# Performance work log

Measured on AMD Instinct MI355X. Metric: run time of the kernel, lower is better.

## Reference

```python
import jax, jax.numpy as jnp
import numpy as np

N_HEADS = 8
N_GROUPS = 32  # GroupNorm groups (normalization(channels) in guided-diffusion)
EPS = 1e-5


def setup_inputs() -> dict:
    key = jax.random.key(0)
    ks = jax.random.split(key, 7)
    b, c, hh, ww = 16, 512, 32, 32
    x = jax.random.normal(ks[0], (b, c, hh, ww), dtype=jnp.float32)
    norm_w = 1.0 + 0.02 * jax.random.normal(ks[1], (c,), dtype=jnp.float32)
    norm_b = 0.02 * jax.random.normal(ks[2], (c,), dtype=jnp.float32)
    # pointwise Conv1d == matmul over channels; note proj_out is zero-initialized
    # in the original, we use random weights so the op is non-trivial.
    qkv_w = jax.random.normal(ks[3], (3 * c, c), dtype=jnp.float32) / np.sqrt(c).astype(np.float32)
    qkv_b = 0.02 * jax.random.normal(ks[4], (3 * c,), dtype=jnp.float32)
    proj_w = jax.random.normal(ks[5], (c, c), dtype=jnp.float32) / np.sqrt(c).astype(np.float32)
    proj_b = 0.02 * jax.random.normal(ks[6], (c,), dtype=jnp.float32)
    return {"x": x, "norm_w": norm_w, "norm_b": norm_b,
            "qkv_w": qkv_w, "qkv_b": qkv_b, "proj_w": proj_w, "proj_b": proj_b}


def reference(x, norm_w, norm_b, qkv_w, qkv_b, proj_w, proj_b):
    b, c, hh, ww = x.shape
    t = hh * ww
    xf = x.reshape(b, c, t)

    # GroupNorm(32, c): normalize over (c//G channels, T) per group
    xg = xf.reshape(b, N_GROUPS, (c // N_GROUPS) * t)
    mu = jnp.mean(xg, axis=-1, keepdims=True)
    var = jnp.var(xg, axis=-1, keepdims=True)
    hn = ((xg - mu) * jax.lax.rsqrt(var + EPS)).reshape(b, c, t)
    hn = hn * norm_w[:, None] + norm_b[:, None]

    # pointwise conv: [b, 3c, t]
    qkv = jnp.einsum('oc,bct->bot', qkv_w, hn) + qkv_b[:, None]

    ch = c // N_HEADS
    qkv = qkv.reshape(b * N_HEADS, 3 * ch, t)
    q, k, v = jnp.split(qkv, 3, axis=1)  # each [b*H, ch, t]
    scale = np.float32(1.0 / np.sqrt(np.sqrt(ch)))
    w = jnp.einsum('bct,bcs->bts', q * scale, k * scale)  # [b*H, t, t]
    w = jax.nn.softmax(w.astype(jnp.float32), axis=-1).astype(qkv.dtype)
    a = jnp.einsum('bts,bcs->bct', w, v).reshape(b, c, t)

    h = jnp.einsum('oc,bct->bot', proj_w, a) + proj_b[:, None]
    return (xf + h).reshape(b, c, hh, ww)
```

## Files before the change

### kernel.cpp

```cpp
#include <hip/hip_runtime.h>

#define TPB 256

typedef __attribute__((ext_vector_type(8))) __bf16 bf16x8;
typedef __attribute__((ext_vector_type(4))) float f32x4;
typedef __attribute__((ext_vector_type(8))) unsigned short u16x8;
typedef __attribute__((ext_vector_type(4))) unsigned short u16x4;
typedef __attribute__((ext_vector_type(4))) unsigned int u32x4;
typedef __attribute__((ext_vector_type(2))) unsigned int u32x2;

typedef __attribute__((address_space(1))) const void gconst_void;
typedef __attribute__((address_space(3))) void lds_void;

__device__ __forceinline__ unsigned short f2bf(float f) {
  unsigned u = __builtin_bit_cast(unsigned, f);
  u += 0x7FFFu + ((u >> 16) & 1u);
  return (unsigned short)(u >> 16);
}

__device__ __forceinline__ float exp2_fast(float x) {
  float r;
  asm("v_exp_f32 %0, %1" : "=v"(r) : "v"(x));
  return r;
}

__device__ __forceinline__ float rcp_fast(float x) {
  float r;
  asm("v_rcp_f32 %0, %1" : "=v"(r) : "v"(x));
  return r;
}

__device__ __forceinline__ unsigned cvt_pk_bf16(float lo, float hi) {
  unsigned r;
  asm("v_cvt_pk_bf16_f32 %0, %1, %2" : "=v"(r) : "v"(lo), "v"(hi));
  return r;
}

__global__ void k_gn_stats(const float* __restrict__ x, float* __restrict__ mu,
                           float* __restrict__ rs) {
  int bg = blockIdx.x;
  const float4* p = reinterpret_cast<const float4*>(x + (size_t)bg * 16384);
  float s = 0.f, ss = 0.f;
  for (int i = threadIdx.x; i < 4096; i += TPB) {
    float4 v = p[i];
    s += v.x + v.y + v.z + v.w;
    ss += v.x * v.x + v.y * v.y + v.z * v.z + v.w * v.w;
  }
#pragma unroll
  for (int off = 1; off < 64; off <<= 1) {
    s += __shfl_xor(s, off, 64);
    ss += __shfl_xor(ss, off, 64);
  }
  __shared__ float rbuf[4][2];
  int wave = threadIdx.x >> 6;
  if ((threadIdx.x & 63) == 0) { rbuf[wave][0] = s; rbuf[wave][1] = ss; }
  __syncthreads();
  if (threadIdx.x == 0) {
    float S = 0.f, SS = 0.f;
    for (int i = 0; i < 4; ++i) { S += rbuf[i][0]; SS += rbuf[i][1]; }
    float m = S * (1.f / 16384.f);
    float var = SS * (1.f / 16384.f) - m * m;
    mu[bg] = m;
    rs[bg] = rsqrtf(var + 1e-5f);
  }
}

__global__ void k_gn_apply(const float* __restrict__ x, const float* __restrict__ mu,
                           const float* __restrict__ rs, const float* __restrict__ nw,
                           const float* __restrict__ nb, unsigned short* __restrict__ hnT) {
  __shared__ unsigned short tile[64][72];
  int b = blockIdx.z, ct = blockIdx.y, tt = blockIdx.x;
  int tid = threadIdx.x;
  int cloc = tid >> 2;
  int tseg = tid & 3;
  int c = ct * 64 + cloc;
  int g = c >> 4;
  float m = mu[b * 32 + g], r = rs[b * 32 + g];
  float a = r * nw[c];
  float bb = nb[c] - m * a;
  const float4* src = reinterpret_cast<const float4*>(
      x + ((size_t)(b * 512 + c)) * 1024 + tt * 64 + tseg * 16);
#pragma unroll
  for (int i = 0; i < 4; ++i) {
    float4 v = src[i];
    int tl = tseg * 16 + i * 4;
    tile[tl + 0][cloc] = f2bf(v.x * a + bb);
    tile[tl + 1][cloc] = f2bf(v.y * a + bb);
    tile[tl + 2][cloc] = f2bf(v.z * a + bb);
    tile[tl + 3][cloc] = f2bf(v.w * a + bb);
  }
  __syncthreads();
  int trow = tid >> 3;
  int cs = (tid & 7) * 8;
#pragma unroll
  for (int p = 0; p < 2; ++p) {
    int tr = trow + p * 32;
    u16x8 v8 = *reinterpret_cast<const u16x8*>(&tile[tr][cs]);
    *reinterpret_cast<u16x8*>(hnT + ((size_t)(b * 1024 + tt * 64 + tr)) * 512 + ct * 64 + cs) = v8;
  }
}

__global__ void k_f32_to_bf16(const float* __restrict__ src, unsigned short* __restrict__ dst,
                              int n4) {
  int i = blockIdx.x * blockDim.x + threadIdx.x;
  if (i < n4) {
    float4 v = reinterpret_cast<const float4*>(src)[i];
    u16x4 o;
    o[0] = f2bf(v.x); o[1] = f2bf(v.y); o[2] = f2bf(v.z); o[3] = f2bf(v.w);
    reinterpret_cast<u16x4*>(dst)[i] = o;
  }
}

__global__ __launch_bounds__(256) void k_qkv_gemm(
    const unsigned short* __restrict__ hnT, const unsigned short* __restrict__ wq,
    const float* __restrict__ qkv_b, unsigned short* __restrict__ Q,
    unsigned short* __restrict__ K, unsigned short* __restrict__ V) {
  __shared__ unsigned short As[2][4096];
  __shared__ unsigned short Bs[2][4096];
  int tid = threadIdx.x;
  int lane = tid & 63, wave = tid >> 6;
  int wm = wave >> 1, wn = wave & 1;
  int g = lane >> 4, li = lane & 15;

  int wg = blockIdx.x;
  int lin = (wg & 7) * 192 + (wg >> 3);
  int bx = lin % 12;
  int tmp = lin / 12;
  int by = tmp & 7;
  int b = tmp >> 3;
  int mbase = by * 128;
  int nbase = bx * 128;

  const unsigned short* Ag = hnT + (size_t)b * 1024 * 512 + (size_t)mbase * 512;
  const unsigned short* Bg = wq + (size_t)nbase * 512;

  int kq = (lane & 3) ^ ((lane >> 3) & 3);
  int rst = wave * 32 + (lane >> 2);
  const char* pA0 = (const char*)Ag + (size_t)rst * 1024 + kq * 16;
  const char* pA1 = pA0 + 16 * 1024;
  const char* pB0 = (const char*)Bg + (size_t)rst * 1024 + kq * 16;
  const char* pB1 = pB0 + 16 * 1024;
  int ldsA0 = wave * 1024, ldsA1 = wave * 1024 + 512;

  int voff = 32 * li + 8 * (g ^ ((li >> 1) & 3));

  f32x4 zero = {0.f, 0.f, 0.f, 0.f};
  f32x4 acc[4][4];
#pragma unroll
  for (int mi = 0; mi < 4; ++mi)
#pragma unroll
    for (int ni = 0; ni < 4; ++ni) acc[mi][ni] = zero;

#define GISSUE(k0, buf)                                                                  \
  do {                                                                                   \
    __builtin_amdgcn_global_load_lds((gconst_void*)(pA0 + (k0) * 2),                     \
                                     (lds_void*)&As[buf][ldsA0], 16, 0, 0);              \
    __builtin_amdgcn_global_load_lds((gconst_void*)(pA1 + (k0) * 2),                     \
                                     (lds_void*)&As[buf][ldsA1], 16, 0, 0);              \
    __builtin_amdgcn_global_load_lds((gconst_void*)(pB0 + (k0) * 2),                     \
                                     (lds_void*)&Bs[buf][ldsA0], 16, 0, 0);              \
    __builtin_amdgcn_global_load_lds((gconst_void*)(pB1 + (k0) * 2),                     \
                                     (lds_void*)&Bs[buf][ldsA1], 16, 0, 0);              \
  } while (0)

  GISSUE(0, 0);
#pragma unroll
  for (int kk = 0; kk < 16; ++kk) {
    asm volatile("s_waitcnt vmcnt(0)" ::: "memory");
    __builtin_amdgcn_s_barrier();
    asm volatile("" ::: "memory");
    if (kk < 15) GISSUE((kk + 1) * 32, (kk + 1) & 1);
    const int cur = kk & 1;
    bf16x8 af[4], bfr[4];
#pragma unroll
    for (int mi = 0; mi < 4; ++mi)
      af[mi] = *reinterpret_cast<const bf16x8*>(&As[cur][wm * 2048 + mi * 512 + voff]);
#pragma unroll
    for (int ni = 0; ni < 4; ++ni)
      bfr[ni] = *reinterpret_cast<const bf16x8*>(&Bs[cur][wn * 2048 + ni * 512 + voff]);
#pragma unroll
    for (int mi = 0; mi < 4; ++mi)
#pragma unroll
      for (int ni = 0; ni < 4; ++ni)
        acc[mi][ni] = __builtin_amdgcn_mfma_f32_16x16x32_bf16(af[mi], bfr[ni], acc[mi][ni], 0, 0, 0);
  }
#undef GISSUE

  const float SCALE = 0.42466090143f;
#pragma unroll
  for (int ni = 0; ni < 4; ++ni) {
    int o = nbase + wn * 64 + ni * 16 + li;
    int h = o / 192;
    int j = o - h * 192;
    int bh = b * 8 + h;
    float bias = qkv_b[o];
#pragma unroll
    for (int mi = 0; mi < 4; ++mi) {
      int t0 = mbase + wm * 64 + mi * 16 + g * 4;
      f32x4 v = acc[mi][ni];
      if (j < 64) {
#pragma unroll
        for (int r = 0; r < 4; ++r)
          Q[((size_t)bh * 1024 + t0 + r) * 64 + j] = f2bf((v[r] + bias) * SCALE);
      } else if (j < 128) {
#pragma unroll
        for (int r = 0; r < 4; ++r)
          K[((size_t)bh * 1024 + t0 + r) * 64 + (j - 64)] = f2bf((v[r] + bias) * SCALE);
      } else {
        u16x4 pv;
#pragma unroll
        for (int r = 0; r < 4; ++r) pv[r] = f2bf(v[r] + bias);
        *reinterpret_cast<u16x4*>(V + ((size_t)bh * 64 + (j - 128)) * 1024 + t0) = pv;
      }
    }
  }
}

__global__ __launch_bounds__(256) void k_attn(
    const unsigned short* __restrict__ Q, const unsigned short* __restrict__ K,
    const unsigned short* __restrict__ V, unsigned short* __restrict__ aT) {
  __shared__ unsigned short Kls[2][4096];
  __shared__ unsigned short Vls[2][4096];
  int tid = threadIdx.x;
  int lane = tid & 63, w = tid >> 6;
  int g = lane >> 4, li = lane & 15;

  int wg = blockIdx.x;
  int lin = (wg & 7) * 128 + (wg >> 3);
  int qt = lin & 7;
  int bh = lin >> 3;
  int tq0 = qt * 128;
  int b = bh >> 3, h = bh & 7;

  const unsigned short* Kg = K + (size_t)bh * 1024 * 64;
  const unsigned short* Vg = V + (size_t)bh * 64 * 1024;

  bf16x8 qf[2][2];
#pragma unroll
  for (int qi = 0; qi < 2; ++qi) {
    int t = tq0 + w * 32 + qi * 16 + li;
    const unsigned short* qp = Q + ((size_t)bh * 1024 + t) * 64 + g * 8;
    qf[qi][0] = *reinterpret_cast<const bf16x8*>(qp);
    qf[qi][1] = *reinterpret_cast<const bf16x8*>(qp + 32);
  }

  int r0 = w * 16 + (lane >> 3);
  int r1 = r0 + 8;
  int h0 = (r0 ^ (r0 >> 2)) & 7;
  int h1 = (r1 ^ (r1 >> 2)) & 7;
  int c0 = ((lane & 7) ^ h0) * 8;
  int c1 = ((lane & 7) ^ h1) * 8;
  const unsigned short* kg0 = Kg + (size_t)r0 * 64 + c0;
  const unsigned short* kg1 = Kg + (size_t)r1 * 64 + c1;
  const unsigned short* vg0 = Vg + (size_t)r0 * 1024 + c0;
  const unsigned short* vg1 = Vg + (size_t)r1 * 1024 + c1;

  int srowK = ((li >> 2) << 3) | (li & 3);

  f32x4 zero = {0.f, 0.f, 0.f, 0.f};
  f32x4 oacc[2][4];
  f32x4 l_acc[2];
#pragma unroll
  for (int qi = 0; qi < 2; ++qi) {
    l_acc[qi] = zero;
#pragma unroll
    for (int nj = 0; nj < 4; ++nj) oacc[qi][nj] = zero;
  }
  u32x4 onesw = {0x3F803F80u, 0x3F803F80u, 0x3F803F80u, 0x3F803F80u};
  bf16x8 ones = __builtin_bit_cast(bf16x8, onesw);

#define ISSUE(tt, pp)                                                                    \
  do {                                                                                   \
    __builtin_amdgcn_global_load_lds((gconst_void*)(kg0 + (size_t)(tt) * 4096),          \
                                     (lds_void*)&Kls[pp][w * 1024], 16, 0, 0);           \
    __builtin_amdgcn_global_load_lds((gconst_void*)(kg1 + (size_t)(tt) * 4096),          \
                                     (lds_void*)&Kls[pp][w * 1024 + 512], 16, 0, 0);     \
    __builtin_amdgcn_global_load_lds((gconst_void*)(vg0 + (size_t)(tt) * 64),            \
                                     (lds_void*)&Vls[pp][w * 1024], 16, 0, 0);           \
    __builtin_amdgcn_global_load_lds((gconst_void*)(vg1 + (size_t)(tt) * 64),            \
                                     (lds_void*)&Vls[pp][w * 1024 + 512], 16, 0, 0);     \
  } while (0)

#define ABODY(cur)                                                                        \
  do {                                                                                    \
    const unsigned short* kbase = &Kls[cur][0];                                           \
    const unsigned short* vbase = &Vls[cur][0];                                           \
    f32x4 sacc[2][4];                                                                     \
    _Pragma("unroll") for (int ni = 0; ni < 4; ++ni) {                                    \
      int rK = ((ni >> 1) << 5) + ((ni & 1) << 2) + srowK;                                \
      int hs = ((rK ^ (rK >> 2)) & 7) << 4;                                               \
      int off0 = ((g << 4)) ^ hs;                                                         \
      int off1 = (64 + (g << 4)) ^ hs;                                                    \
      bf16x8 kf0 = *reinterpret_cast<const bf16x8*>(&kbase[rK * 64 + (off0 >> 1)]);       \
      bf16x8 kf1 = *reinterpret_cast<const bf16x8*>(&kbase[rK * 64 + (off1 >> 1)]);       \
      _Pragma("unroll") for (int qi = 0; qi < 2; ++qi) {                                  \
        f32x4 s0 = __builtin_amdgcn_mfma_f32_16x16x32_bf16(kf0, qf[qi][0], zero, 0, 0, 0);\
        sacc[qi][ni] = __builtin_amdgcn_mfma_f32_16x16x32_bf16(kf1, qf[qi][1], s0, 0, 0, 0);\
      }                                                                                   \
    }                                                                                     \
    bf16x8 pfrag[2][2];                                                                   \
    _Pragma("unroll") for (int qi = 0; qi < 2; ++qi) {                                    \
      _Pragma("unroll") for (int ni = 0; ni < 4; ++ni)                                    \
        _Pragma("unroll") for (int r = 0; r < 4; ++r)                                     \
          sacc[qi][ni][r] = exp2_fast(sacc[qi][ni][r]);                                   \
      _Pragma("unroll") for (int kk = 0; kk < 2; ++kk) {                                  \
        u32x4 pw;                                                                         \
        pw[0] = cvt_pk_bf16(sacc[qi][2 * kk][0], sacc[qi][2 * kk][1]);                    \
        pw[1] = cvt_pk_bf16(sacc[qi][2 * kk][2], sacc[qi][2 * kk][3]);                    \
        pw[2] = cvt_pk_bf16(sacc[qi][2 * kk + 1][0], sacc[qi][2 * kk + 1][1]);            \
        pw[3] = cvt_pk_bf16(sacc[qi][2 * kk + 1][2], sacc[qi][2 * kk + 1][3]);            \
        pfrag[qi][kk] = __builtin_bit_cast(bf16x8, pw);                                   \
      }                                                                                   \
      l_acc[qi] = __builtin_amdgcn_mfma_f32_16x16x32_bf16(ones, pfrag[qi][0], l_acc[qi], 0, 0, 0); \
      l_acc[qi] = __builtin_amdgcn_mfma_f32_16x16x32_bf16(ones, pfrag[qi][1], l_acc[qi], 0, 0, 0); \
    }                                                                                     \
    _Pragma("unroll") for (int nj = 0; nj < 4; ++nj) {                                    \
      int rV = nj * 16 + li;                                                              \
      int hv = ((rV ^ (rV >> 2)) & 7) << 4;                                               \
      int off0 = ((g << 4)) ^ hv;                                                         \
      int off1 = (64 + (g << 4)) ^ hv;                                                    \
      bf16x8 vf0 = *reinterpret_cast<const bf16x8*>(&vbase[rV * 64 + (off0 >> 1)]);       \
      bf16x8 vf1 = *reinterpret_cast<const bf16x8*>(&vbase[rV * 64 + (off1 >> 1)]);       \
      _Pragma("unroll") for (int qi = 0; qi < 2; ++qi) {                                  \
        oacc[qi][nj] = __builtin_amdgcn_mfma_f32_16x16x32_bf16(vf0, pfrag[qi][0], oacc[qi][nj], 0, 0, 0); \
        oacc[qi][nj] = __builtin_amdgcn_mfma_f32_16x16x32_bf16(vf1, pfrag[qi][1], oacc[qi][nj], 0, 0, 0); \
      }                                                                                   \
    }                                                                                     \
  } while (0)

  ISSUE(0, 0);
  for (int t = 0; t < 16; ++t) {
    asm volatile("s_waitcnt vmcnt(0)" ::: "memory");
    __builtin_amdgcn_s_barrier();
    asm volatile("" ::: "memory");
    if (t < 15) ISSUE(t + 1, (t + 1) & 1);
    ABODY(t & 1);
  }
#undef ISSUE
#undef ABODY

#pragma unroll
  for (int qi = 0; qi < 2; ++qi) {
    float inv = rcp_fast(l_acc[qi][0]);
    int t = tq0 + w * 32 + qi * 16 + li;
#pragma unroll
    for (int nj = 0; nj < 4; ++nj) {
      u32x2 ov;
      ov[0] = cvt_pk_bf16(oacc[qi][nj][0] * inv, oacc[qi][nj][1] * inv);
      ov[1] = cvt_pk_bf16(oacc[qi][nj][2] * inv, oacc[qi][nj][3] * inv);
      *reinterpret_cast<u32x2*>(aT + ((size_t)b * 1024 + t) * 512 + h * 64 + nj * 16 + g * 4) = ov;
    }
  }
}

__global__ __launch_bounds__(256) void k_proj_gemm(
    const unsigned short* __restrict__ aT, const unsigned short* __restrict__ wp,
    const float* __restrict__ proj_b, const float* __restrict__ x,
    float* __restrict__ out) {
  __shared__ unsigned short As[2][4096];
  __shared__ unsigned short Bs[2][4096];
  int tid = threadIdx.x;
  int lane = tid & 63, wave = tid >> 6;
  int wm = wave >> 1, wn = wave & 1;
  int g = lane >> 4, li = lane & 15;

  int wg = blockIdx.x;
  int lin = (wg & 7) * 64 + (wg >> 3);
  int bx = lin & 7;
  int tmp = lin >> 3;
  int by = tmp & 3;
  int b = tmp >> 2;
  int mbase = by * 128;
  int nbase = bx * 128;

  const unsigned short* Ag = wp + (size_t)mbase * 512;
  const unsigned short* Bg = aT + (size_t)b * 1024 * 512 + (size_t)nbase * 512;

  int kq = (lane & 3) ^ ((lane >> 3) & 3);
  int rst = wave * 32 + (lane >> 2);
  const char* pA0 = (const char*)Ag + (size_t)rst * 1024 + kq * 16;
  const char* pA1 = pA0 + 16 * 1024;
  const char* pB0 = (const char*)Bg + (size_t)rst * 1024 + kq * 16;
  const char* pB1 = pB0 + 16 * 1024;
  int ldsA0 = wave * 1024, ldsA1 = wave * 1024 + 512;

  int voff = 32 * li + 8 * (g ^ ((li >> 1) & 3));

  f32x4 zero = {0.f, 0.f, 0.f, 0.f};
  f32x4 acc[4][4];
#pragma unroll
  for (int mi = 0; mi < 4; ++mi)
#pragma unroll
    for (int ni = 0; ni < 4; ++ni) acc[mi][ni] = zero;

#define GISSUE(k0, buf)                                                                  \
  do {                                                                                   \
    __builtin_amdgcn_global_load_lds((gconst_void*)(pA0 + (k0) * 2),                     \
                                     (lds_void*)&As[buf][ldsA0], 16, 0, 0);              \
    __builtin_amdgcn_global_load_lds((gconst_void*)(pA1 + (k0) * 2),                     \
                                     (lds_void*)&As[buf][ldsA1], 16, 0, 0);              \
    __builtin_amdgcn_global_load_lds((gconst_void*)(pB0 + (k0) * 2),                     \
                                     (lds_void*)&Bs[buf][ldsA0], 16, 0, 0);              \
    __builtin_amdgcn_global_load_lds((gconst_void*)(pB1 + (k0) * 2),                     \
                                     (lds_void*)&Bs[buf][ldsA1], 16, 0, 0);              \
  } while (0)

  GISSUE(0, 0);
#pragma unroll
  for (int kk = 0; kk < 16; ++kk) {
    asm volatile("s_waitcnt vmcnt(0)" ::: "memory");
    __builtin_amdgcn_s_barrier();
    asm volatile("" ::: "memory");
    if (kk < 15) GISSUE((kk + 1) * 32, (kk + 1) & 1);
    const int cur = kk & 1;
    bf16x8 af[4], bfr[4];
#pragma unroll
    for (int mi = 0; mi < 4; ++mi)
      af[mi] = *reinterpret_cast<const bf16x8*>(&As[cur][wm * 2048 + mi * 512 + voff]);
#pragma unroll
    for (int ni = 0; ni < 4; ++ni)
      bfr[ni] = *reinterpret_cast<const bf16x8*>(&Bs[cur][wn * 2048 + ni * 512 + voff]);
#pragma unroll
    for (int mi = 0; mi < 4; ++mi)
#pragma unroll
      for (int ni = 0; ni < 4; ++ni)
        acc[mi][ni] = __builtin_amdgcn_mfma_f32_16x16x32_bf16(af[mi], bfr[ni], acc[mi][ni], 0, 0, 0);
  }
#undef GISSUE

#pragma unroll
  for (int mi = 0; mi < 4; ++mi) {
#pragma unroll
    for (int ni = 0; ni < 4; ++ni) {
      int t = nbase + wn * 64 + ni * 16 + li;
      f32x4 v = acc[mi][ni];
#pragma unroll
      for (int r = 0; r < 4; ++r) {
        int o = mbase + wm * 64 + mi * 16 + g * 4 + r;
        size_t idx = ((size_t)(b * 512 + o)) * 1024 + t;
        out[idx] = v[r] + proj_b[o] + x[idx];
      }
    }
  }
}

extern "C" void kernel_launch(void* const* d_in, const int* in_sizes, int n_in,
                              void* d_out, int out_size, void* d_ws, size_t ws_size,
                              hipStream_t stream) {
  (void)in_sizes; (void)n_in; (void)out_size; (void)ws_size;
  const float* x = (const float*)d_in[0];
  const float* norm_w = (const float*)d_in[1];
  const float* norm_b = (const float*)d_in[2];
  const float* qkv_w = (const float*)d_in[3];
  const float* qkv_b = (const float*)d_in[4];
  const float* proj_w = (const float*)d_in[5];
  const float* proj_b = (const float*)d_in[6];
  float* out = (float*)d_out;

  char* ws = (char*)d_ws;
  size_t off = 0;
  float* mu = (float*)(ws + off); off += 2048;
  float* rs = (float*)(ws + off); off += 2048;
  unsigned short* hnT = (unsigned short*)(ws + off); off += (size_t)16 * 1024 * 512 * 2;
  unsigned short* wqb = (unsigned short*)(ws + off); off += (size_t)1536 * 512 * 2;
  unsigned short* wpb = (unsigned short*)(ws + off); off += (size_t)512 * 512 * 2;
  unsigned short* Qb = (unsigned short*)(ws + off); off += (size_t)128 * 1024 * 64 * 2;
  unsigned short* Kb = (unsigned short*)(ws + off); off += (size_t)128 * 1024 * 64 * 2;
  unsigned short* Vb = (unsigned short*)(ws + off); off += (size_t)128 * 1024 * 64 * 2;

  k_gn_stats<<<512, TPB, 0, stream>>>(x, mu, rs);
  k_gn_apply<<<dim3(16, 8, 16), TPB, 0, stream>>>(x, mu, rs, norm_w, norm_b, hnT);
  k_f32_to_bf16<<<(786432 / 4 + TPB - 1) / TPB, TPB, 0, stream>>>(qkv_w, wqb, 786432 / 4);
  k_f32_to_bf16<<<(262144 / 4 + TPB - 1) / TPB, TPB, 0, stream>>>(proj_w, wpb, 262144 / 4);
  k_qkv_gemm<<<1536, TPB, 0, stream>>>(hnT, wqb, qkv_b, Qb, Kb, Vb);
  k_attn<<<1024, TPB, 0, stream>>>(Qb, Kb, Vb, hnT );
  k_proj_gemm<<<512, TPB, 0, stream>>>(hnT, wpb, proj_b, x, out);
}
```

Measured before the change: 141.6 us.

## Pre-pack GEMM operands into MFMA fragment layout and load directly to registers

Activations (hnT, attention output) and weights are now written in a tiled layout matching the MFMA 16x16x32 fragment order, so each lane reads its 16-byte fragment straight from global memory. Both GEMMs drop the LDS double buffer, barriers and global_load_lds staging in favour of a register ping-pong prefetch, with launch bounds raised to allow more resident waves. This targets LDS traffic and barrier stalls, but each wave now loads its own operand copies from global/L2 with no sharing across waves through LDS. The attention kernel also adds an lgkmcnt wait before its barrier.

```diff
diff --git a/kernel.cpp b/kernel.cpp
--- a/kernel.cpp
+++ b/kernel.cpp
@@ -35,6 +35,7 @@
   asm("v_cvt_pk_bf16_f32 %0, %1, %2" : "=v"(r) : "v"(lo), "v"(hi));
   return r;
 }
+
 
 __global__ void k_gn_stats(const float* __restrict__ x, float* __restrict__ mu,
                            float* __restrict__ rs) {
@@ -96,27 +97,48 @@
   for (int p = 0; p < 2; ++p) {
     int tr = trow + p * 32;
     u16x8 v8 = *reinterpret_cast<const u16x8*>(&tile[tr][cs]);
-    *reinterpret_cast<u16x8*>(hnT + ((size_t)(b * 1024 + tt * 64 + tr)) * 512 + ct * 64 + cs) = v8;
-  }
-}
-
-__global__ void k_f32_to_bf16(const float* __restrict__ src, unsigned short* __restrict__ dst,
-                              int n4) {
+    int t = tt * 64 + tr;
+    int cc = ct * 64 + cs;
+    size_t dst = (size_t)b * 524288 + (size_t)(t >> 4) * 8192 + (size_t)(cc >> 5) * 512 +
+                 ((cc >> 3) & 3) * 128 + (t & 15) * 8;
+    *reinterpret_cast<u16x8*>(hnT + dst) = v8;
+  }
+}
+
+__global__ void k_pack_w(const float* __restrict__ src, unsigned short* __restrict__ dst,
+                         int nchunks) {
   int i = blockIdx.x * blockDim.x + threadIdx.x;
-  if (i < n4) {
-    float4 v = reinterpret_cast<const float4*>(src)[i];
-    u16x4 o;
-    o[0] = f2bf(v.x); o[1] = f2bf(v.y); o[2] = f2bf(v.z); o[3] = f2bf(v.w);
-    reinterpret_cast<u16x4*>(dst)[i] = o;
-  }
-}
-
-__global__ __launch_bounds__(256) void k_qkv_gemm(
+  if (i >= nchunks) return;
+  int r = i >> 6, k8 = i & 63;
+  const float4* s = reinterpret_cast<const float4*>(src + (size_t)r * 512 + k8 * 8);
+  float4 v0 = s[0], v1 = s[1];
+  u16x8 o;
+  o[0] = f2bf(v0.x); o[1] = f2bf(v0.y); o[2] = f2bf(v0.z); o[3] = f2bf(v0.w);
+  o[4] = f2bf(v1.x); o[5] = f2bf(v1.y); o[6] = f2bf(v1.z); o[7] = f2bf(v1.w);
+  size_t d = (size_t)(r >> 4) * 8192 + (size_t)(k8 >> 2) * 512 + (k8 & 3) * 128 + (r & 15) * 8;
+  *reinterpret_cast<u16x8*>(dst + d) = o;
+}
+
+#define MFMAS(AF, BF)                                                                     \
+  do {                                                                                    \
+    _Pragma("unroll") for (int mi = 0; mi < 4; ++mi)                                      \
+      _Pragma("unroll") for (int ni = 0; ni < 4; ++ni)                                    \
+        acc[mi][ni] =                                                                     \
+            __builtin_amdgcn_mfma_f32_16x16x32_bf16(AF[mi], BF[ni], acc[mi][ni], 0, 0, 0);\
+  } while (0)
+
+#define LOADT(DA, DB, kb)                                                                 \
+  do {                                                                                    \
+    _Pragma("unroll") for (int mi = 0; mi < 4; ++mi)                                      \
+      DA[mi] = *reinterpret_cast<const bf16x8*>(pA + (size_t)mi * 8192 + (kb) * 512);     \
+    _Pragma("unroll") for (int ni = 0; ni < 4; ++ni)                                      \
+      DB[ni] = *reinterpret_cast<const bf16x8*>(pB + (size_t)ni * 8192 + (kb) * 512);     \
+  } while (0)
+
+__global__ __launch_bounds__(256, 4) void k_qkv_gemm(
     const unsigned short* __restrict__ hnT, const unsigned short* __restrict__ wq,
     const float* __restrict__ qkv_b, unsigned short* __restrict__ Q,
     unsigned short* __restrict__ K, unsigned short* __restrict__ V) {
-  __shared__ unsigned short As[2][4096];
-  __shared__ unsigned short Bs[2][4096];
   int tid = threadIdx.x;
   int lane = tid & 63, wave = tid >> 6;
   int wm = wave >> 1, wn = wave & 1;
@@ -131,18 +153,9 @@
   int mbase = by * 128;
   int nbase = bx * 128;
 
-  const unsigned short* Ag = hnT + (size_t)b * 1024 * 512 + (size_t)mbase * 512;
-  const unsigned short* Bg = wq + (size_t)nbase * 512;
-
-  int kq = (lane & 3) ^ ((lane >> 3) & 3);
-  int rst = wave * 32 + (lane >> 2);
-  const char* pA0 = (const char*)Ag + (size_t)rst * 1024 + kq * 16;
-  const char* pA1 = pA0 + 16 * 1024;
-  const char* pB0 = (const char*)Bg + (size_t)rst * 1024 + kq * 16;
-  const char* pB1 = pB0 + 16 * 1024;
-  int ldsA0 = wave * 1024, ldsA1 = wave * 1024 + 512;
-
-  int voff = 32 * li + 8 * (g ^ ((li >> 1) & 3));
+  const unsigned short* pA =
+      hnT + (size_t)b * 524288 + (size_t)((mbase + wm * 64) >> 4) * 8192 + lane * 8;
+  const unsigned short* pB = wq + (size_t)((nbase + wn * 64) >> 4) * 8192 + lane * 8;
 
   f32x4 zero = {0.f, 0.f, 0.f, 0.f};
   f32x4 acc[4][4];
@@ -151,40 +164,15 @@
 #pragma unroll
     for (int ni = 0; ni < 4; ++ni) acc[mi][ni] = zero;
 
-#define GISSUE(k0, buf)                                                                  \
-  do {                                                                                   \
-    __builtin_amdgcn_global_load_lds((gconst_void*)(pA0 + (k0) * 2),                     \
-                                     (lds_void*)&As[buf][ldsA0], 16, 0, 0);              \
-    __builtin_amdgcn_global_load_lds((gconst_void*)(pA1 + (k0) * 2),                     \
-                                     (lds_void*)&As[buf][ldsA1], 16, 0, 0);              \
-    __builtin_amdgcn_global_load_lds((gconst_void*)(pB0 + (k0) * 2),                     \
-                                     (lds_void*)&Bs[buf][ldsA0], 16, 0, 0);              \
-    __builtin_amdgcn_global_load_lds((gconst_void*)(pB1 + (k0) * 2),                     \
-                                     (lds_void*)&Bs[buf][ldsA1], 16, 0, 0);              \
-  } while (0)
-
-  GISSUE(0, 0);
-#pragma unroll
-  for (int kk = 0; kk < 16; ++kk) {
-    asm volatile("s_waitcnt vmcnt(0)" ::: "memory");
-    __builtin_amdgcn_s_barrier();
-    asm volatile("" ::: "memory");
-    if (kk < 15) GISSUE((kk + 1) * 32, (kk + 1) & 1);
-    const int cur = kk & 1;
-    bf16x8 af[4], bfr[4];
-#pragma unroll
-    for (int mi = 0; mi < 4; ++mi)
-      af[mi] = *reinterpret_cast<const bf16x8*>(&As[cur][wm * 2048 + mi * 512 + voff]);
-#pragma unroll
-    for (int ni = 0; ni < 4; ++ni)
-      bfr[ni] = *reinterpret_cast<const bf16x8*>(&Bs[cur][wn * 2048 + ni * 512 + voff]);
-#pragma unroll
-    for (int mi = 0; mi < 4; ++mi)
-#pragma unroll
-      for (int ni = 0; ni < 4; ++ni)
-        acc[mi][ni] = __builtin_amdgcn_mfma_f32_16x16x32_bf16(af[mi], bfr[ni], acc[mi][ni], 0, 0, 0);
-  }
-#undef GISSUE
+  bf16x8 a0[4], b0[4], a1[4], b1[4];
+  LOADT(a0, b0, 0);
+#pragma unroll
+  for (int kb = 0; kb < 16; kb += 2) {
+    if (kb + 1 < 16) LOADT(a1, b1, kb + 1);
+    MFMAS(a0, b0);
+    if (kb + 2 < 16) LOADT(a0, b0, kb + 2);
+    MFMAS(a1, b1);
+  }
 
   const float SCALE = 0.42466090143f;
 #pragma unroll
@@ -330,7 +318,7 @@
 
   ISSUE(0, 0);
   for (int t = 0; t < 16; ++t) {
-    asm volatile("s_waitcnt vmcnt(0)" ::: "memory");
+    asm volatile("s_waitcnt vmcnt(0) lgkmcnt(0)" ::: "memory");
     __builtin_amdgcn_s_barrier();
     asm volatile("" ::: "memory");
     if (t < 15) ISSUE(t + 1, (t + 1) & 1);
@@ -345,20 +333,21 @@
     int t = tq0 + w * 32 + qi * 16 + li;
 #pragma unroll
     for (int nj = 0; nj < 4; ++nj) {
+      int c = h * 64 + nj * 16 + g * 4;
       u32x2 ov;
       ov[0] = cvt_pk_bf16(oacc[qi][nj][0] * inv, oacc[qi][nj][1] * inv);
       ov[1] = cvt_pk_bf16(oacc[qi][nj][2] * inv, oacc[qi][nj][3] * inv);
-      *reinterpret_cast<u32x2*>(aT + ((size_t)b * 1024 + t) * 512 + h * 64 + nj * 16 + g * 4) = ov;
+      size_t dst = (size_t)b * 524288 + (size_t)(t >> 4) * 8192 + (size_t)(c >> 5) * 512 +
+                   ((c >> 3) & 3) * 128 + (t & 15) * 8 + (c & 7);
+      *reinterpret_cast<u32x2*>(aT + dst) = ov;
     }
   }
 }
 
-__global__ __launch_bounds__(256) void k_proj_gemm(
+__global__ __launch_bounds__(256, 4) void k_proj_gemm(
     const unsigned short* __restrict__ aT, const unsigned short* __restrict__ wp,
     const float* __restrict__ proj_b, const float* __restrict__ x,
     float* __restrict__ out) {
-  __shared__ unsigned short As[2][4096];
-  __shared__ unsigned short Bs[2][4096];
   int tid = threadIdx.x;
   int lane = tid & 63, wave = tid >> 6;
   int wm = wave >> 1, wn = wave & 1;
@@ -373,18 +362,9 @@
   int mbase = by * 128;
   int nbase = bx * 128;
 
-  const unsigned short* Ag = wp + (size_t)mbase * 512;
-  const unsigned short* Bg = aT + (size_t)b * 1024 * 512 + (size_t)nbase * 512;
-
-  int kq = (lane & 3) ^ ((lane >> 3) & 3);
-  int rst = wave * 32 + (lane >> 2);
-  const char* pA0 = (const char*)Ag + (size_t)rst * 1024 + kq * 16;
-  const char* pA1 = pA0 + 16 * 1024;
-  const char* pB0 = (const char*)Bg + (size_t)rst * 1024 + kq * 16;
-  const char* pB1 = pB0 + 16 * 1024;
-  int ldsA0 = wave * 1024, ldsA1 = wave * 1024 + 512;
-
-  int voff = 32 * li + 8 * (g ^ ((li >> 1) & 3));
+  const unsigned short* pA = wp + (size_t)((mbase + wm * 64) >> 4) * 8192 + lane * 8;
+  const unsigned short* pB =
+      aT + (size_t)b * 524288 + (size_t)((nbase + wn * 64) >> 4) * 8192 + lane * 8;
 
   f32x4 zero = {0.f, 0.f, 0.f, 0.f};
   f32x4 acc[4][4];
@@ -393,40 +373,15 @@
 #pragma unroll
     for (int ni = 0; ni < 4; ++ni) acc[mi][ni] = zero;
 
-#define GISSUE(k0, buf)                                                                  \
-  do {                                                                                   \
-    __builtin_amdgcn_global_load_lds((gconst_void*)(pA0 + (k0) * 2),                     \
-                                     (lds_void*)&As[buf][ldsA0], 16, 0, 0);              \
-    __builtin_amdgcn_global_load_lds((gconst_void*)(pA1 + (k0) * 2),                     \
-                                     (lds_void*)&As[buf][ldsA1], 16, 0, 0);              \
-    __builtin_amdgcn_global_load_lds((gconst_void*)(pB0 + (k0) * 2),                     \
-                                     (lds_void*)&Bs[buf][ldsA0], 16, 0, 0);              \
-    __builtin_amdgcn_global_load_lds((gconst_void*)(pB1 + (k0) * 2),                     \
-                                     (lds_void*)&Bs[buf][ldsA1], 16, 0, 0);              \
-  } while (0)
-
-  GISSUE(0, 0);
-#pragma unroll
-  for (int kk = 0; kk < 16; ++kk) {
-    asm volatile("s_waitcnt vmcnt(0)" ::: "memory");
-    __builtin_amdgcn_s_barrier();
-    asm volatile("" ::: "memory");
-    if (kk < 15) GISSUE((kk + 1) * 32, (kk + 1) & 1);
-    const int cur = kk & 1;
-    bf16x8 af[4], bfr[4];
-#pragma unroll
-    for (int mi = 0; mi < 4; ++mi)
-      af[mi] = *reinterpret_cast<const bf16x8*>(&As[cur][wm * 2048 + mi * 512 + voff]);
-#pragma unroll
-    for (int ni = 0; ni < 4; ++ni)
-      bfr[ni] = *reinterpret_cast<const bf16x8*>(&Bs[cur][wn * 2048 + ni * 512 + voff]);
-#pragma unroll
-    for (int mi = 0; mi < 4; ++mi)
-#pragma unroll
-      for (int ni = 0; ni < 4; ++ni)
-        acc[mi][ni] = __builtin_amdgcn_mfma_f32_16x16x32_bf16(af[mi], bfr[ni], acc[mi][ni], 0, 0, 0);
-  }
-#undef GISSUE
+  bf16x8 a0[4], b0[4], a1[4], b1[4];
+  LOADT(a0, b0, 0);
+#pragma unroll
+  for (int kb = 0; kb < 16; kb += 2) {
+    if (kb + 1 < 16) LOADT(a1, b1, kb + 1);
+    MFMAS(a0, b0);
+    if (kb + 2 < 16) LOADT(a0, b0, kb + 2);
+    MFMAS(a1, b1);
+  }
 
 #pragma unroll
   for (int mi = 0; mi < 4; ++mi) {
@@ -470,8 +425,8 @@
 
   k_gn_stats<<<512, TPB, 0, stream>>>(x, mu, rs);
   k_gn_apply<<<dim3(16, 8, 16), TPB, 0, stream>>>(x, mu, rs, norm_w, norm_b, hnT);
-  k_f32_to_bf16<<<(786432 / 4 + TPB - 1) / TPB, TPB, 0, stream>>>(qkv_w, wqb, 786432 / 4);
-  k_f32_to_bf16<<<(262144 / 4 + TPB - 1) / TPB, TPB, 0, stream>>>(proj_w, wpb, 262144 / 4);
+  k_pack_w<<<(98304 + TPB - 1) / TPB, TPB, 0, stream>>>(qkv_w, wqb, 98304);
+  k_pack_w<<<(32768 + TPB - 1) / TPB, TPB, 0, stream>>>(proj_w, wpb, 32768);
   k_qkv_gemm<<<1536, TPB, 0, stream>>>(hnT, wqb, qkv_b, Qb, Kb, Vb);
   k_attn<<<1024, TPB, 0, stream>>>(Qb, Kb, Vb, hnT );
   k_proj_gemm<<<512, TPB, 0, stream>>>(hnT, wpb, proj_b, x, out);
```

Result: slower. 200.2 us (+41.3%).
